# Kernel optimization log

Hardware: AMD Instinct MI355X
Metric: run time of the kernel (lower is better)

## Reference

```python
import jax, jax.numpy as jnp
import numpy as np

H, D = 8, 16          # heads, per-head dim (hidden=128)
N_NEWS, N_INTER, F_IN, C_OUT = 30000, 60000, 768, 4
HID = H * D


def setup_inputs() -> dict:
    key = jax.random.key(0)
    ks = jax.random.split(key, 20)
    s = lambda i, shape, sc=0.05: (jax.random.normal(ks[i], shape, dtype=jnp.float32) * sc)
    inp = {
        "x_news": jax.random.normal(ks[0], (N_NEWS, F_IN), dtype=jnp.float32),
        "x_inter": jax.random.normal(ks[1], (N_INTER, F_IN), dtype=jnp.float32),
        "edge_nn": jax.random.randint(ks[2], (2, 480000), 0, N_NEWS),
        "edge_in": jax.random.randint(ks[3], (2, 960000), 0, N_NEWS),
        # per-node-type input projections (HANConv.proj)
        "W_news": s(4, (F_IN, HID)), "b_news": jnp.zeros((HID,), jnp.float32),
        "W_inter": s(5, (F_IN, HID)), "b_inter": jnp.zeros((HID,), jnp.float32),
        # per-edge-type node-level attention vectors (lin_src / lin_dst)
        "a_src_nn": s(6, (H, D), 0.2), "a_dst_nn": s(7, (H, D), 0.2),
        "a_src_in": s(8, (H, D), 0.2), "a_dst_in": s(9, (H, D), 0.2),
        # semantic-level attention (k_lin, q)
        "Wk": s(10, (HID, HID)), "bk": jnp.zeros((HID,), jnp.float32),
        "q": s(11, (HID,), 0.2),
        # output head
        "W_out": s(12, (HID, C_OUT)), "b_out": jnp.zeros((C_OUT,), jnp.float32),
    }
    return inp


def _han_conv(h_src, h_dst, edge, a_src, a_dst, n_dst):
    # node-level (GAT-style) attention for one edge type
    asrc = (h_src * a_src).sum(-1)            # [Ns, H]
    adst = (h_dst * a_dst).sum(-1)            # [Nd, H]
    src, dst = edge[0], edge[1]
    e = jax.nn.leaky_relu(asrc[src] + adst[dst], negative_slope=0.2)   # [E, H]
    m = jax.ops.segment_max(e, dst, num_segments=n_dst)                # [Nd, H]
    m = jnp.where(jnp.isfinite(m), m, jnp.float32(0))
    ex = jnp.exp(e - m[dst])
    denom = jax.ops.segment_sum(ex, dst, num_segments=n_dst)
    alpha = ex / (denom[dst] + jnp.float32(1e-16))                     # [E, H]
    out = jax.ops.segment_sum(h_src[src] * alpha[:, :, None], dst, num_segments=n_dst)
    return jax.nn.relu(out.reshape(n_dst, H * D))                      # [Nd, HID]


def reference(x_news, x_inter, edge_nn, edge_in,
              W_news, b_news, W_inter, b_inter,
              a_src_nn, a_dst_nn, a_src_in, a_dst_in,
              Wk, bk, q, W_out, b_out):
    # per-node-type projection, reshape to heads
    h_news = (x_news @ W_news + b_news).reshape(-1, H, D)
    h_inter = (x_inter @ W_inter + b_inter).reshape(-1, H, D)
    # per-edge-type node-level attention conv (dst is always 'news')
    out_nn = _han_conv(h_news, h_news, edge_nn, a_src_nn, a_dst_nn, N_NEWS)
    out_in = _han_conv(h_inter, h_news, edge_in, a_src_in, a_dst_in, N_NEWS)
    # semantic-level attention across metapaths
    outs = jnp.stack([out_nn, out_in])                       # [2, N, HID]
    score = (q * jnp.tanh(outs @ Wk + bk).mean(axis=1)).sum(-1)   # [2]
    beta = jax.nn.softmax(score, axis=0)
    fused = (beta[:, None, None] * outs).sum(0)              # [N, HID]
    # head: ELU + (eval-mode dropout = identity) + Linear
    return jax.nn.elu(fused) @ W_out + b_out
```

## Files before the change

### kernel.cpp

```cpp
#include <hip/hip_runtime.h>
#include <hip/hip_bf16.h>

#define N_NODES   30000
#define F_IN      768
#define HID       128
#define NHEAD     8
#define C_OUT     4

typedef short short8_t __attribute__((ext_vector_type(8)));
typedef float float4_t __attribute__((ext_vector_type(4)));

__device__ __forceinline__ float b2f(short u) {
    union { unsigned int i; float f; } v;
    v.i = ((unsigned int)(unsigned short)u) << 16;
    return v.f;
}
__device__ __forceinline__ short f2s(float f) {
    __hip_bfloat16 h = __float2bfloat16(f);
    short s; __builtin_memcpy(&s, &h, 2); return s;
}

#define OFF_H_NEWS      0UL
#define OFF_H_INTER     7680000UL
#define OFF_OUT_NN      15360000UL
#define OFF_OUT_IN      23040000UL
#define OFF_ASRC_NN     30720000UL
#define OFF_ADST_NN     31680000UL
#define OFF_ASRC_IN     32640000UL
#define OFF_ADST_IN     33600000UL
#define OFF_WT_NEWS     34560000UL
#define OFF_WT_INTER    34756608UL
#define OFF_RS_NN       34953216UL
#define OFF_RS_IN       35073280UL
#define OFF_SORT_NN     35193344UL
#define OFF_SORT_IN     37113344UL
#define OFF_ZERO        40953344UL
#define OFF_DEG_NN      40953344UL
#define OFF_FILL_NN     41073408UL
#define OFF_DEG_IN      41193472UL
#define OFF_FILL_IN     41313536UL
#define OFF_SSUM        41433600UL
#define ZERO_BYTES      481280UL
#define OFF_BETA        41434624UL
#define OFF_FLAG        41434632UL
#define OFF_CPAR        41434640UL
#define OFF_WKT         41470496UL

#define CP_B_NEWS  0
#define CP_B_INTER 128
#define CP_ASRC_NN 256
#define CP_ADST_NN 384
#define CP_ASRC_IN 512
#define CP_ADST_IN 640
#define CP_WK      768
#define CP_BK      17152
#define CP_Q       17280
#define CP_WOUT    17408
#define CP_BOUT    17920
#define CP_TOTAL   17924

__global__ void detect_dtype(const unsigned int* __restrict__ x, int* __restrict__ flag) {
    __shared__ int cnt_s;
    if (threadIdx.x == 0) cnt_s = 0;
    __syncthreads();
    int sane = 0;
    for (int i = threadIdx.x; i < 16384; i += 256) {
        unsigned int lo = x[i] & 0xFFFFu;
        unsigned int ex = (lo >> 7) & 0xFFu;
        if ((ex >= 107u && ex <= 147u) || lo == 0u || lo == 0x8000u) sane++;
    }
    atomicAdd(&cnt_s, sane);
    __syncthreads();
    if (threadIdx.x == 0) *flag = (cnt_s > 8192) ? 1 : 0;
}

struct SmallParams {
    const void* src[11];
    int n[11];
    int dstoff[11];
};
__global__ void convert_small(SmallParams sp, short* __restrict__ dst,
                              const int* __restrict__ flag) {
    bool isbf = (*flag != 0);
    int idx = blockIdx.x * 256 + threadIdx.x;
    for (int s = 0; s < 11; ++s) {
        if (idx < sp.n[s]) {
            short v = isbf ? ((const short*)sp.src[s])[idx]
                           : f2s(((const float*)sp.src[s])[idx]);
            dst[sp.dstoff[s] + idx] = v;
            return;
        }
        idx -= sp.n[s];
    }
}

__global__ void transpose_w2(const void* __restrict__ Wn, const void* __restrict__ Wi,
                             short* __restrict__ WtN, short* __restrict__ WtI,
                             const int* __restrict__ flag) {
    bool isbf = (*flag != 0);
    const void* Wraw = blockIdx.y ? Wi : Wn;
    short* Wt        = blockIdx.y ? WtI : WtN;
    int idx = blockIdx.x * 256 + threadIdx.x;
    if (idx < F_IN * HID) {
        int n = idx / F_IN;
        int k = idx - n * F_IN;
        short v = isbf ? ((const short*)Wraw)[k * HID + n]
                       : f2s(((const float*)Wraw)[k * HID + n]);
        Wt[idx] = v;
    }
}

__global__ void transpose_wk(const short* __restrict__ cp, short* __restrict__ wkT) {
    int idx = blockIdx.x * 256 + threadIdx.x;
    if (idx < HID * HID) {
        int j = idx >> 7;
        int k = idx & 127;
        wkT[idx] = cp[CP_WK + k * HID + j];
    }
}

#define BK   32
#define LDK  40

__global__ __launch_bounds__(256) void proj_gemm2(
    const void* __restrict__ Xn, const void* __restrict__ Xi,
    const short* __restrict__ WtN, const short* __restrict__ WtI,
    const short* __restrict__ cp,
    short* __restrict__ Hn, short* __restrict__ Hi,
    int M, const int* __restrict__ flag)
{
    __shared__ __align__(16) short As[64 * LDK];
    __shared__ __align__(16) short Bs[128 * LDK];

    const bool isbf = (*flag != 0);
    const void* Xraw = blockIdx.y ? Xi : Xn;
    const short* Wt  = blockIdx.y ? WtI : WtN;
    const short* bias = cp + (blockIdx.y ? CP_B_INTER : CP_B_NEWS);
    short* Hout      = blockIdx.y ? Hi : Hn;

    int m0   = blockIdx.x * 64;
    int tid  = threadIdx.x;
    int lane = tid & 63;
    int wid  = tid >> 6;
    int quad = lane >> 4;
    int lm   = lane & 15;

    float4_t acc[8];
    #pragma unroll
    for (int c = 0; c < 8; ++c) acc[c] = (float4_t){0.f, 0.f, 0.f, 0.f};

    int sr  = tid >> 2;
    int skp = (tid & 3) * 8;

    for (int k0 = 0; k0 < F_IN; k0 += BK) {
        __syncthreads();
        {
            int gm = m0 + sr; if (gm >= M) gm = M - 1;
            short8_t av;
            if (isbf) {
                av = *(const short8_t*)((const short*)Xraw + (size_t)gm * F_IN + k0 + skp);
            } else {
                const float* xf = (const float*)Xraw + (size_t)gm * F_IN + k0 + skp;
                float4_t f0 = *(const float4_t*)xf;
                float4_t f1 = *(const float4_t*)(xf + 4);
                av[0] = f2s(f0[0]); av[1] = f2s(f0[1]); av[2] = f2s(f0[2]); av[3] = f2s(f0[3]);
                av[4] = f2s(f1[0]); av[5] = f2s(f1[1]); av[6] = f2s(f1[2]); av[7] = f2s(f1[3]);
            }
            *(short8_t*)(&As[sr * LDK + skp]) = av;
        }
        #pragma unroll
        for (int rep = 0; rep < 2; ++rep) {
            int r = sr + rep * 64;
            short8_t bv = *(const short8_t*)(Wt + (size_t)r * F_IN + k0 + skp);
            *(short8_t*)(&Bs[r * LDK + skp]) = bv;
        }
        __syncthreads();

        short8_t bfrag[8];
        #pragma unroll
        for (int c = 0; c < 8; ++c)
            bfrag[c] = *(const short8_t*)(&Bs[(c * 16 + lm) * LDK + quad * 8]);
        short8_t afrag = *(const short8_t*)(&As[(wid * 16 + lm) * LDK + quad * 8]);
        #pragma unroll
        for (int c = 0; c < 8; ++c)
            acc[c] = __builtin_amdgcn_mfma_f32_16x16x32_bf16(afrag, bfrag[c], acc[c], 0, 0, 0);
    }

    #pragma unroll
    for (int c = 0; c < 8; ++c)
        #pragma unroll
        for (int r = 0; r < 4; ++r) {
            int row = wid * 16 + quad * 4 + r;
            int gm = m0 + row;
            if (gm < M) {
                int col = c * 16 + lm;
                Hout[(size_t)gm * HID + col] = f2s(acc[c][r] + b2f(bias[col]));
            }
        }
}

__global__ __launch_bounds__(128) void head_dots(
    const short* __restrict__ Hnews, const short* __restrict__ Hinter,
    const short* __restrict__ cp,
    float* __restrict__ asrc_nn, float* __restrict__ adst_nn,
    float* __restrict__ asrc_in, float* __restrict__ adst_in)
{
    int n = blockIdx.x, tid = threadIdx.x;
    int h = tid >> 4, d = tid & 15;
    float hv  = b2f(Hnews[(size_t)n * HID + tid]);
    float hv2 = b2f(Hinter[(size_t)n * HID + tid]);
    float v0 = hv  * b2f(cp[CP_ASRC_NN + tid]);
    float v1 = hv  * b2f(cp[CP_ADST_NN + tid]);
    float v2 = hv2 * b2f(cp[CP_ASRC_IN + tid]);
    float v3 = hv  * b2f(cp[CP_ADST_IN + tid]);
    #pragma unroll
    for (int off = 8; off; off >>= 1) {
        v0 += __shfl_down(v0, off, 16);
        v1 += __shfl_down(v1, off, 16);
        v2 += __shfl_down(v2, off, 16);
        v3 += __shfl_down(v3, off, 16);
    }
    if (d == 0) {
        asrc_nn[n * NHEAD + h] = v0;
        adst_nn[n * NHEAD + h] = v1;
        asrc_in[n * NHEAD + h] = v2;
        adst_in[n * NHEAD + h] = v3;
    }
}

__global__ void count_deg2(const int* __restrict__ dnn, int Enn,
                           const int* __restrict__ din, int Ein,
                           int* __restrict__ deg_nn, int* __restrict__ deg_in) {
    int i = blockIdx.x * 256 + threadIdx.x;
    if (i < Enn) {
        int d = dnn[i];
        if (d >= 0 && d < N_NODES) atomicAdd(&deg_nn[d], 1);
    } else {
        int j = i - Enn;
        if (j < Ein) {
            int d = din[j];
            if (d >= 0 && d < N_NODES) atomicAdd(&deg_in[d], 1);
        }
    }
}

__global__ __launch_bounds__(256) void prefix_scan2(
    const int* __restrict__ deg_nn, int* __restrict__ rs_nn,
    const int* __restrict__ deg_in, int* __restrict__ rs_in, int n)
{
    const int* deg = blockIdx.x ? deg_in : deg_nn;
    int* row_start = blockIdx.x ? rs_in : rs_nn;
    __shared__ int psum[256];
    int tid = threadIdx.x;
    int chunk = (n + 255) / 256;
    int lo = tid * chunk;
    int hi = lo + chunk; if (hi > n) hi = n; if (lo > n) lo = n;
    int s = 0;
    for (int i = lo; i < hi; ++i) s += deg[i];
    psum[tid] = s;
    __syncthreads();
    for (int off = 1; off < 256; off <<= 1) {
        int v = (tid >= off) ? psum[tid - off] : 0;
        __syncthreads();
        psum[tid] += v;
        __syncthreads();
    }
    int base = tid ? psum[tid - 1] : 0;
    for (int i = lo; i < hi; ++i) { row_start[i] = base; base += deg[i]; }
    if (tid == 255) row_start[n] = psum[255];
}

__global__ void scatter_edges2(const int* __restrict__ enn, int Enn,
                               const int* __restrict__ ein, int Ein,
                               const int* __restrict__ rs_nn, int* __restrict__ fill_nn,
                               int* __restrict__ sort_nn,
                               const int* __restrict__ rs_in, int* __restrict__ fill_in,
                               int* __restrict__ sort_in) {
    int i = blockIdx.x * 256 + threadIdx.x;
    if (i < Enn) {
        int d = enn[Enn + i];
        if (d >= 0 && d < N_NODES) {
            int pos = rs_nn[d] + atomicAdd(&fill_nn[d], 1);
            if (pos >= 0 && pos < Enn) sort_nn[pos] = enn[i];
        }
    } else {
        int j = i - Enn;
        if (j < Ein) {
            int d = ein[Ein + j];
            if (d >= 0 && d < N_NODES) {
                int pos = rs_in[d] + atomicAdd(&fill_in[d], 1);
                if (pos >= 0 && pos < Ein) sort_in[pos] = ein[j];
            }
        }
    }
}

__global__ __launch_bounds__(256) void aggregate2(
    const short* __restrict__ Hnn, const short* __restrict__ Hin,
    const float* __restrict__ asrc_nn, const float* __restrict__ adst_nn,
    const float* __restrict__ asrc_in, const float* __restrict__ adst_in,
    const int* __restrict__ rs_nn, const int* __restrict__ rs_in,
    const int* __restrict__ sort_nn, const int* __restrict__ sort_in,
    short* __restrict__ out_nn, short* __restrict__ out_in)
{
    int tid = threadIdx.x, w = tid >> 6, lane = tid & 63;
    int type = blockIdx.y;
    const short* H    = type ? Hin : Hnn;
    const float* asrc = type ? asrc_in : asrc_nn;
    const float* adst = type ? adst_in : adst_nn;
    const int*   rs   = type ? rs_in : rs_nn;
    const int*   ss   = type ? sort_in : sort_nn;
    short* outb       = type ? out_in : out_nn;

    int dn = blockIdx.x * 4 + w;
    int start = rs[dn], end = rs[dn + 1];
    int head = lane >> 3;
    float adv = adst[dn * NHEAD + head];

    float den = 0.f, a0 = 0.f, a1 = 0.f;
    for (int base = start; base < end; base += 64) {
        int nb = end - base; if (nb > 64) nb = 64;
        int myidx = 0;
        if (base + lane < end) myidx = ss[base + lane];
        for (int j = 0; j < nb; ++j) {
            int s = __shfl(myidx, j, 64);
            s = (s < 0) ? 0 : (s >= N_NODES ? N_NODES - 1 : s);
            float e = asrc[s * NHEAD + head] + adv;
            e = fmaxf(e, 0.2f * e);
            e = fminf(e, 80.f);
            float ex = __expf(e);
            unsigned int hv = *(const unsigned int*)(H + (size_t)s * HID + lane * 2);
            den += ex;
            a0 += ex * b2f((short)(hv & 0xFFFFu));
            a1 += ex * b2f((short)(hv >> 16));
        }
    }
    float inv = 1.f / (den + 1e-16f);
    unsigned int lo16 = (unsigned short)f2s(fmaxf(a0 * inv, 0.f));
    unsigned int hi16 = (unsigned short)f2s(fmaxf(a1 * inv, 0.f));
    *(unsigned int*)(outb + (size_t)dn * HID + lane * 2) = lo16 | (hi16 << 16);
}

__global__ __launch_bounds__(256) void score_mfma(
    const short* __restrict__ out_nn, const short* __restrict__ out_in,
    const short* __restrict__ wkT, const short* __restrict__ cp,
    float* __restrict__ Ssum)
{
    __shared__ float col_s[HID];
    int tid  = threadIdx.x;
    int lane = tid & 63;
    int wid  = tid >> 6;
    int quad = lane >> 4;
    int lm   = lane & 15;
    const short* src = blockIdx.y ? out_in : out_nn;
    int m0 = blockIdx.x * 128;

    if (tid < HID) col_s[tid] = 0.f;
    __syncthreads();

    float4_t acc[2][8];
    #pragma unroll
    for (int i = 0; i < 2; ++i)
        #pragma unroll
        for (int c = 0; c < 8; ++c)
            acc[i][c] = (float4_t){0.f, 0.f, 0.f, 0.f};

    #pragma unroll
    for (int kc = 0; kc < 4; ++kc) {
        short8_t bfrag[8];
        #pragma unroll
        for (int c = 0; c < 8; ++c)
            bfrag[c] = *(const short8_t*)(wkT + (c * 16 + lm) * HID + kc * 32 + quad * 8);
        #pragma unroll
        for (int i = 0; i < 2; ++i) {
            int gm = m0 + wid * 32 + i * 16 + lm;
            if (gm >= N_NODES) gm = N_NODES - 1;
            short8_t afrag = *(const short8_t*)(src + (size_t)gm * HID + kc * 32 + quad * 8);
            #pragma unroll
            for (int c = 0; c < 8; ++c)
                acc[i][c] = __builtin_amdgcn_mfma_f32_16x16x32_bf16(afrag, bfrag[c], acc[i][c], 0, 0, 0);
        }
    }

    #pragma unroll
    for (int c = 0; c < 8; ++c) {
        int col = c * 16 + lm;
        float bkc = b2f(cp[CP_BK + col]);
        float lsum = 0.f;
        #pragma unroll
        for (int i = 0; i < 2; ++i)
            #pragma unroll
            for (int r = 0; r < 4; ++r) {
                int node = m0 + wid * 32 + i * 16 + quad * 4 + r;
                if (node < N_NODES) {
                    float a = acc[i][c][r] + bkc;
                    a = fminf(fmaxf(a, -15.f), 15.f);
                    float t = __expf(2.f * a);
                    lsum += (t - 1.f) / (t + 1.f);
                }
            }
        float v = lsum;
        v += __shfl_down(v, 32, 64);
        v += __shfl_down(v, 16, 64);
        if (quad == 0) atomicAdd(&col_s[col], v);
    }
    __syncthreads();
    if (tid < HID) atomicAdd(&Ssum[blockIdx.y * HID + tid], col_s[tid]);
}

__global__ __launch_bounds__(64) void beta_kernel(
    const float* __restrict__ Ssum, const short* __restrict__ cp, float* __restrict__ beta)
{
    int lane = threadIdx.x;
    float q0 = b2f(cp[CP_Q + lane]), q1 = b2f(cp[CP_Q + lane + 64]);
    float s0 = q0 * Ssum[lane] + q1 * Ssum[lane + 64];
    float s1 = q0 * Ssum[128 + lane] + q1 * Ssum[192 + lane];
    #pragma unroll
    for (int off = 32; off; off >>= 1) {
        s0 += __shfl_down(s0, off, 64);
        s1 += __shfl_down(s1, off, 64);
    }
    if (lane == 0) {
        float sc0 = s0 / (float)N_NODES;
        float sc1 = s1 / (float)N_NODES;
        float mx = fmaxf(sc0, sc1);
        float e0 = __expf(sc0 - mx), e1 = __expf(sc1 - mx);
        float inv = 1.f / (e0 + e1);
        beta[0] = e0 * inv;
        beta[1] = e1 * inv;
    }
}

__global__ __launch_bounds__(128) void final_out(
    const short* __restrict__ out_nn, const short* __restrict__ out_in,
    const float* __restrict__ beta, const short* __restrict__ cp,
    void* __restrict__ Yraw, const int* __restrict__ flag)
{
    __shared__ float partial[2][C_OUT];
    bool isbf = (*flag != 0);
    int n = blockIdx.x, tid = threadIdx.x, lane = tid & 63, w = tid >> 6;
    float b0 = beta[0], b1 = beta[1];
    float f = b0 * b2f(out_nn[(size_t)n * HID + tid]) + b1 * b2f(out_in[(size_t)n * HID + tid]);
    float e = (f > 0.f) ? f : expm1f(f);
    float p[C_OUT];
    #pragma unroll
    for (int c = 0; c < C_OUT; ++c) p[c] = e * b2f(cp[CP_WOUT + tid * C_OUT + c]);
    #pragma unroll
    for (int off = 32; off; off >>= 1)
        #pragma unroll
        for (int c = 0; c < C_OUT; ++c) p[c] += __shfl_down(p[c], off, 64);
    if (lane == 0)
        #pragma unroll
        for (int c = 0; c < C_OUT; ++c) partial[w][c] = p[c];
    __syncthreads();
    if (tid < C_OUT) {
        float r = partial[0][tid] + partial[1][tid] + b2f(cp[CP_BOUT + tid]);
        if (isbf) ((__hip_bfloat16*)Yraw)[n * C_OUT + tid] = __float2bfloat16(r);
        else      ((float*)Yraw)[n * C_OUT + tid] = r;
    }
}

extern "C" void kernel_launch(void* const* d_in, const int* in_sizes, int n_in,
                              void* d_out, int out_size, void* d_ws, size_t ws_size,
                              hipStream_t stream) {
    const void* x_news  = d_in[0];
    const void* x_inter = d_in[1];
    const int*  edge_nn = (const int*)d_in[2];
    const int*  edge_in = (const int*)d_in[3];

    int E_nn = in_sizes[2] / 2;
    int E_in = in_sizes[3] / 2;

    char* ws = (char*)d_ws;
    short* h_news  = (short*)(ws + OFF_H_NEWS);
    short* h_inter = (short*)(ws + OFF_H_INTER);
    short* out_nn  = (short*)(ws + OFF_OUT_NN);
    short* out_in  = (short*)(ws + OFF_OUT_IN);
    float* asrc_nn = (float*)(ws + OFF_ASRC_NN);
    float* adst_nn = (float*)(ws + OFF_ADST_NN);
    float* asrc_in = (float*)(ws + OFF_ASRC_IN);
    float* adst_in = (float*)(ws + OFF_ADST_IN);
    short* wt_news  = (short*)(ws + OFF_WT_NEWS);
    short* wt_inter = (short*)(ws + OFF_WT_INTER);
    int* rs_nn   = (int*)(ws + OFF_RS_NN);
    int* rs_in   = (int*)(ws + OFF_RS_IN);
    int* sort_nn = (int*)(ws + OFF_SORT_NN);
    int* sort_in = (int*)(ws + OFF_SORT_IN);
    int* deg_nn  = (int*)(ws + OFF_DEG_NN);
    int* fill_nn = (int*)(ws + OFF_FILL_NN);
    int* deg_in  = (int*)(ws + OFF_DEG_IN);
    int* fill_in = (int*)(ws + OFF_FILL_IN);
    float* Ssum  = (float*)(ws + OFF_SSUM);
    float* beta  = (float*)(ws + OFF_BETA);
    int*   flag  = (int*)(ws + OFF_FLAG);
    short* cp    = (short*)(ws + OFF_CPAR);
    short* wkT   = (short*)(ws + OFF_WKT);

    hipMemsetAsync(ws + OFF_ZERO, 0, ZERO_BYTES, stream);

    detect_dtype<<<1, 256, 0, stream>>>((const unsigned int*)x_news, flag);

    SmallParams sp;
    const int srcidx[11] = {5, 7, 8, 9, 10, 11, 12, 13, 14, 15, 16};
    const int ns[11]     = {128, 128, 128, 128, 128, 128, 16384, 128, 128, 512, 4};
    const int doff[11]   = {CP_B_NEWS, CP_B_INTER, CP_ASRC_NN, CP_ADST_NN, CP_ASRC_IN,
                            CP_ADST_IN, CP_WK, CP_BK, CP_Q, CP_WOUT, CP_BOUT};
    for (int i = 0; i < 11; ++i) { sp.src[i] = d_in[srcidx[i]]; sp.n[i] = ns[i]; sp.dstoff[i] = doff[i]; }
    convert_small<<<(CP_TOTAL + 255) / 256, 256, 0, stream>>>(sp, cp, flag);

    transpose_wk<<<(HID * HID + 255) / 256, 256, 0, stream>>>(cp, wkT);

    transpose_w2<<<dim3((F_IN * HID + 255) / 256, 2), 256, 0, stream>>>(
        d_in[4], d_in[6], wt_news, wt_inter, flag);

    proj_gemm2<<<dim3((N_NODES + 63) / 64, 2), 256, 0, stream>>>(
        x_news, x_inter, wt_news, wt_inter, cp, h_news, h_inter, N_NODES, flag);

    head_dots<<<N_NODES, 128, 0, stream>>>(h_news, h_inter, cp,
        asrc_nn, adst_nn, asrc_in, adst_in);

    count_deg2<<<(E_nn + E_in + 255) / 256, 256, 0, stream>>>(
        edge_nn + E_nn, E_nn, edge_in + E_in, E_in, deg_nn, deg_in);

    prefix_scan2<<<2, 256, 0, stream>>>(deg_nn, rs_nn, deg_in, rs_in, N_NODES);

    scatter_edges2<<<(E_nn + E_in + 255) / 256, 256, 0, stream>>>(
        edge_nn, E_nn, edge_in, E_in, rs_nn, fill_nn, sort_nn, rs_in, fill_in, sort_in);

    aggregate2<<<dim3(N_NODES / 4, 2), 256, 0, stream>>>(
        h_news, h_inter, asrc_nn, adst_nn, asrc_in, adst_in,
        rs_nn, rs_in, sort_nn, sort_in, out_nn, out_in);

    score_mfma<<<dim3((N_NODES + 127) / 128, 2), 256, 0, stream>>>(out_nn, out_in, wkT, cp, Ssum);
    beta_kernel<<<1, 64, 0, stream>>>(Ssum, cp, beta);

    final_out<<<N_NODES, 128, 0, stream>>>(out_nn, out_in, beta, cp, d_out, flag);
}
```

Before: 703.8 us.

## Fuse prep, projection, head dots and degree count; merge beta into score

```diff
diff --git a/kernel.cpp b/kernel.cpp
--- a/kernel.cpp
+++ b/kernel.cpp
@@ -9,6 +9,7 @@
 
 typedef short short8_t __attribute__((ext_vector_type(8)));
 typedef float float4_t __attribute__((ext_vector_type(4)));
+typedef int   int4_t   __attribute__((ext_vector_type(4)));
 
 __device__ __forceinline__ float b2f(short u) {
     union { unsigned int i; float f; } v;
@@ -40,11 +41,12 @@
 #define OFF_DEG_IN      41193472UL
 #define OFF_FILL_IN     41313536UL
 #define OFF_SSUM        41433600UL
-#define ZERO_BYTES      481280UL
-#define OFF_BETA        41434624UL
-#define OFF_FLAG        41434632UL
-#define OFF_CPAR        41434640UL
-#define OFF_WKT         41470496UL
+#define OFF_CNT         41434624UL
+#define ZERO_BYTES      481296UL
+#define OFF_BETA        41434640UL
+#define OFF_FLAG        41434648UL
+#define OFF_CPAR        41434656UL
+#define OFF_WKT         41470512UL
 
 #define CP_B_NEWS  0
 #define CP_B_INTER 128
@@ -59,12 +61,23 @@
 #define CP_BOUT    17920
 #define CP_TOTAL   17924
 
+#define PREP_CONV_BLOCKS 7
+#define PREP_TW_BLOCKS   384
+#define PREP_WK_BLOCKS   64
+#define PREP_ZERO_BLOCKS 118
+#define PREP_B0 PREP_CONV_BLOCKS
+#define PREP_B1 (PREP_B0 + 2*PREP_TW_BLOCKS)
+#define PREP_B2 (PREP_B1 + PREP_WK_BLOCKS)
+#define PREP_TOTAL (PREP_B2 + PREP_ZERO_BLOCKS)
+
+#define GEMM_BX 469
+
 __global__ void detect_dtype(const unsigned int* __restrict__ x, int* __restrict__ flag) {
     __shared__ int cnt_s;
     if (threadIdx.x == 0) cnt_s = 0;
     __syncthreads();
     int sane = 0;
-    for (int i = threadIdx.x; i < 16384; i += 256) {
+    for (int i = threadIdx.x; i < 16384; i += 1024) {
         unsigned int lo = x[i] & 0xFFFFu;
         unsigned int ex = (lo >> 7) & 0xFFu;
         if ((ex >= 107u && ex <= 147u) || lo == 0u || lo == 0x8000u) sane++;
@@ -75,70 +88,100 @@
 }
 
 struct SmallParams {
-    const void* src[11];
-    int n[11];
-    int dstoff[11];
+    const void* src[10];
+    int n[10];
+    int dstoff[10];
 };
-__global__ void convert_small(SmallParams sp, short* __restrict__ dst,
-                              const int* __restrict__ flag) {
-    bool isbf = (*flag != 0);
-    int idx = blockIdx.x * 256 + threadIdx.x;
-    for (int s = 0; s < 11; ++s) {
-        if (idx < sp.n[s]) {
-            short v = isbf ? ((const short*)sp.src[s])[idx]
-                           : f2s(((const float*)sp.src[s])[idx]);
-            dst[sp.dstoff[s] + idx] = v;
-            return;
-        }
-        idx -= sp.n[s];
-    }
-}
-
-__global__ void transpose_w2(const void* __restrict__ Wn, const void* __restrict__ Wi,
-                             short* __restrict__ WtN, short* __restrict__ WtI,
-                             const int* __restrict__ flag) {
-    bool isbf = (*flag != 0);
-    const void* Wraw = blockIdx.y ? Wi : Wn;
-    short* Wt        = blockIdx.y ? WtI : WtN;
-    int idx = blockIdx.x * 256 + threadIdx.x;
-    if (idx < F_IN * HID) {
-        int n = idx / F_IN;
-        int k = idx - n * F_IN;
-        short v = isbf ? ((const short*)Wraw)[k * HID + n]
-                       : f2s(((const float*)Wraw)[k * HID + n]);
-        Wt[idx] = v;
-    }
-}
-
-__global__ void transpose_wk(const short* __restrict__ cp, short* __restrict__ wkT) {
-    int idx = blockIdx.x * 256 + threadIdx.x;
-    if (idx < HID * HID) {
-        int j = idx >> 7;
-        int k = idx & 127;
-        wkT[idx] = cp[CP_WK + k * HID + j];
+
+__global__ void prep(SmallParams sp, short* __restrict__ cp,
+                     const void* __restrict__ Wn, const void* __restrict__ Wi,
+                     const void* __restrict__ Wkraw,
+                     short* __restrict__ WtN, short* __restrict__ WtI,
+                     short* __restrict__ wkT,
+                     char* __restrict__ zbase,
+                     const int* __restrict__ flag) {
+    const bool isbf = (*flag != 0);
+    int b = blockIdx.x, tid = threadIdx.x;
+    if (b < PREP_B0) {
+        int idx = b * 256 + tid;
+        for (int s = 0; s < 10; ++s) {
+            if (idx < sp.n[s]) {
+                short v = isbf ? ((const short*)sp.src[s])[idx]
+                               : f2s(((const float*)sp.src[s])[idx]);
+                cp[sp.dstoff[s] + idx] = v;
+                return;
+            }
+            idx -= sp.n[s];
+        }
+    } else if (b < PREP_B1) {
+        int bb = b - PREP_B0;
+        int ty = bb >= PREP_TW_BLOCKS;
+        const void* Wraw = ty ? Wi : Wn;
+        short* Wt        = ty ? WtI : WtN;
+        int idx = (bb - ty * PREP_TW_BLOCKS) * 256 + tid;
+        if (idx < F_IN * HID) {
+            int n = idx / F_IN;
+            int k = idx - n * F_IN;
+            Wt[idx] = isbf ? ((const short*)Wraw)[k * HID + n]
+                           : f2s(((const float*)Wraw)[k * HID + n]);
+        }
+    } else if (b < PREP_B2) {
+        int idx = (b - PREP_B1) * 256 + tid;
+        if (idx < HID * HID) {
+            int j = idx >> 7;
+            int k = idx & 127;
+            wkT[idx] = isbf ? ((const short*)Wkraw)[k * HID + j]
+                            : f2s(((const float*)Wkraw)[k * HID + j]);
+        }
+    } else {
+        size_t off = ((size_t)(b - PREP_B2) * 256 + tid) * 16;
+        if (off < ZERO_BYTES) *(int4_t*)(zbase + off) = (int4_t){0, 0, 0, 0};
     }
 }
 
 #define BK   32
 #define LDK  40
 
-__global__ __launch_bounds__(256) void proj_gemm2(
+__global__ __launch_bounds__(256) void proj_count(
     const void* __restrict__ Xn, const void* __restrict__ Xi,
     const short* __restrict__ WtN, const short* __restrict__ WtI,
     const short* __restrict__ cp,
     short* __restrict__ Hn, short* __restrict__ Hi,
+    float* __restrict__ asrc_nn, float* __restrict__ adst_nn,
+    float* __restrict__ asrc_in, float* __restrict__ adst_in,
+    const int* __restrict__ dnn, int Enn,
+    const int* __restrict__ din, int Ein,
+    int* __restrict__ deg_nn, int* __restrict__ deg_in,
     int M, const int* __restrict__ flag)
 {
     __shared__ __align__(16) short As[64 * LDK];
     __shared__ __align__(16) short Bs[128 * LDK];
 
+    int b = blockIdx.x;
+    if (b >= 2 * GEMM_BX) {
+        int i = (b - 2 * GEMM_BX) * 256 + threadIdx.x;
+        if (i < Enn) {
+            int d = dnn[i];
+            if ((unsigned)d < (unsigned)N_NODES) atomicAdd(&deg_nn[d], 1);
+        } else {
+            int j = i - Enn;
+            if (j < Ein) {
+                int d = din[j];
+                if ((unsigned)d < (unsigned)N_NODES) atomicAdd(&deg_in[d], 1);
+            }
+        }
+        return;
+    }
+
     const bool isbf = (*flag != 0);
-    const void* Xraw = blockIdx.y ? Xi : Xn;
-    const short* Wt  = blockIdx.y ? WtI : WtN;
-    const short* bias = cp + (blockIdx.y ? CP_B_INTER : CP_B_NEWS);
-    short* Hout      = blockIdx.y ? Hi : Hn;
-
-    int m0   = blockIdx.x * 64;
+    int ty = b >= GEMM_BX;
+    int bx = b - ty * GEMM_BX;
+    const void* Xraw = ty ? Xi : Xn;
+    const short* Wt  = ty ? WtI : WtN;
+    const short* bias = cp + (ty ? CP_B_INTER : CP_B_NEWS);
+    short* Hout      = ty ? Hi : Hn;
+
+    int m0   = bx * 64;
     int tid  = threadIdx.x;
     int lane = tid & 63;
     int wid  = tid >> 6;
@@ -186,60 +229,43 @@
             acc[c] = __builtin_amdgcn_mfma_f32_16x16x32_bf16(afrag, bfrag[c], acc[c], 0, 0, 0);
     }
 
+    const short* aw0 = cp + (ty ? CP_ASRC_IN : CP_ASRC_NN);
+    const short* aw1 = cp + CP_ADST_NN;
+    const short* aw2 = cp + CP_ADST_IN;
+
     #pragma unroll
-    for (int c = 0; c < 8; ++c)
+    for (int c = 0; c < 8; ++c) {
+        int col = c * 16 + lm;
+        float bv = b2f(bias[col]);
+        float w0 = b2f(aw0[col]);
+        float w1 = b2f(aw1[col]);
+        float w2 = b2f(aw2[col]);
         #pragma unroll
         for (int r = 0; r < 4; ++r) {
-            int row = wid * 16 + quad * 4 + r;
-            int gm = m0 + row;
-            if (gm < M) {
-                int col = c * 16 + lm;
-                Hout[(size_t)gm * HID + col] = f2s(acc[c][r] + b2f(bias[col]));
+            int gm = m0 + wid * 16 + quad * 4 + r;
+            bool ok = gm < M;
+            float hval = acc[c][r] + bv;
+            if (ok) Hout[(size_t)gm * HID + col] = f2s(hval);
+            if (ty == 0) {
+                float d0 = hval * w0, d1 = hval * w1, d2 = hval * w2;
+                #pragma unroll
+                for (int off = 1; off < 16; off <<= 1) {
+                    d0 += __shfl_xor(d0, off, 16);
+                    d1 += __shfl_xor(d1, off, 16);
+                    d2 += __shfl_xor(d2, off, 16);
+                }
+                if (lm == 0 && ok) {
+                    asrc_nn[gm * NHEAD + c] = d0;
+                    adst_nn[gm * NHEAD + c] = d1;
+                    adst_in[gm * NHEAD + c] = d2;
+                }
+            } else {
+                float d0 = hval * w0;
+                #pragma unroll
+                for (int off = 1; off < 16; off <<= 1)
+                    d0 += __shfl_xor(d0, off, 16);
+                if (lm == 0 && ok) asrc_in[gm * NHEAD + c] = d0;
             }
-        }
-}
-
-__global__ __launch_bounds__(128) void head_dots(
-    const short* __restrict__ Hnews, const short* __restrict__ Hinter,
-    const short* __restrict__ cp,
-    float* __restrict__ asrc_nn, float* __restrict__ adst_nn,
-    float* __restrict__ asrc_in, float* __restrict__ adst_in)
-{
-    int n = blockIdx.x, tid = threadIdx.x;
-    int h = tid >> 4, d = tid & 15;
-    float hv  = b2f(Hnews[(size_t)n * HID + tid]);
-    float hv2 = b2f(Hinter[(size_t)n * HID + tid]);
-    float v0 = hv  * b2f(cp[CP_ASRC_NN + tid]);
-    float v1 = hv  * b2f(cp[CP_ADST_NN + tid]);
-    float v2 = hv2 * b2f(cp[CP_ASRC_IN + tid]);
-    float v3 = hv  * b2f(cp[CP_ADST_IN + tid]);
-    #pragma unroll
-    for (int off = 8; off; off >>= 1) {
-        v0 += __shfl_down(v0, off, 16);
-        v1 += __shfl_down(v1, off, 16);
-        v2 += __shfl_down(v2, off, 16);
-        v3 += __shfl_down(v3, off, 16);
-    }
-    if (d == 0) {
-        asrc_nn[n * NHEAD + h] = v0;
-        adst_nn[n * NHEAD + h] = v1;
-        asrc_in[n * NHEAD + h] = v2;
-        adst_in[n * NHEAD + h] = v3;
-    }
-}
-
-__global__ void count_deg2(const int* __restrict__ dnn, int Enn,
-                           const int* __restrict__ din, int Ein,
-                           int* __restrict__ deg_nn, int* __restrict__ deg_in) {
-    int i = blockIdx.x * 256 + threadIdx.x;
-    if (i < Enn) {
-        int d = dnn[i];
-        if (d >= 0 && d < N_NODES) atomicAdd(&deg_nn[d], 1);
-    } else {
-        int j = i - Enn;
-        if (j < Ein) {
-            int d = din[j];
-            if (d >= 0 && d < N_NODES) atomicAdd(&deg_in[d], 1);
         }
     }
 }
@@ -316,23 +342,48 @@
     int start = rs[dn], end = rs[dn + 1];
     int head = lane >> 3;
     float adv = adst[dn * NHEAD + head];
+    const short* Hl = H + lane * 2;
 
     float den = 0.f, a0 = 0.f, a1 = 0.f;
     for (int base = start; base < end; base += 64) {
         int nb = end - base; if (nb > 64) nb = 64;
         int myidx = 0;
-        if (base + lane < end) myidx = ss[base + lane];
-        for (int j = 0; j < nb; ++j) {
-            int s = __shfl(myidx, j, 64);
-            s = (s < 0) ? 0 : (s >= N_NODES ? N_NODES - 1 : s);
-            float e = asrc[s * NHEAD + head] + adv;
-            e = fmaxf(e, 0.2f * e);
-            e = fminf(e, 80.f);
-            float ex = __expf(e);
-            unsigned int hv = *(const unsigned int*)(H + (size_t)s * HID + lane * 2);
-            den += ex;
-            a0 += ex * b2f((short)(hv & 0xFFFFu));
-            a1 += ex * b2f((short)(hv >> 16));
+        if (base + lane < end) {
+            int t = ss[base + lane];
+            myidx = (t < 0) ? 0 : (t >= N_NODES ? N_NODES - 1 : t);
+        }
+        int j = 0;
+        for (; j + 2 <= nb; j += 2) {
+            int s0 = __shfl(myidx, j, 64);
+            int s1 = __shfl(myidx, j + 1, 64);
+            float v0 = asrc[s0 * NHEAD + head];
+            float v1 = asrc[s1 * NHEAD + head];
+            unsigned int q0 = *(const unsigned int*)(Hl + (size_t)s0 * HID);
+            unsigned int q1 = *(const unsigned int*)(Hl + (size_t)s1 * HID);
+            float e0 = v0 + adv, e1 = v1 + adv;
+            e0 = fmaxf(e0, 0.2f * e0); e1 = fmaxf(e1, 0.2f * e1);
+            e0 = fminf(e0, 80.f);      e1 = fminf(e1, 80.f);
+            float x0 = __expf(e0), x1 = __expf(e1);
+            union { unsigned int u; float f; } cl0, ch0, cl1, ch1;
+            cl0.u = q0 << 16; ch0.u = q0 & 0xFFFF0000u;
+            cl1.u = q1 << 16; ch1.u = q1 & 0xFFFF0000u;
+            den += x0; den += x1;
+            a0 = fmaf(x0, cl0.f, a0); a0 = fmaf(x1, cl1.f, a0);
+            a1 = fmaf(x0, ch0.f, a1); a1 = fmaf(x1, ch1.f, a1);
+        }
+        if (j < nb) {
+            int s0 = __shfl(myidx, j, 64);
+            float v0 = asrc[s0 * NHEAD + head];
+            unsigned int q0 = *(const unsigned int*)(Hl + (size_t)s0 * HID);
+            float e0 = v0 + adv;
+            e0 = fmaxf(e0, 0.2f * e0);
+            e0 = fminf(e0, 80.f);
+            float x0 = __expf(e0);
+            union { unsigned int u; float f; } cl0, ch0;
+            cl0.u = q0 << 16; ch0.u = q0 & 0xFFFF0000u;
+            den += x0;
+            a0 = fmaf(x0, cl0.f, a0);
+            a1 = fmaf(x0, ch0.f, a1);
         }
     }
     float inv = 1.f / (den + 1e-16f);
@@ -344,9 +395,11 @@
 __global__ __launch_bounds__(256) void score_mfma(
     const short* __restrict__ out_nn, const short* __restrict__ out_in,
     const short* __restrict__ wkT, const short* __restrict__ cp,
-    float* __restrict__ Ssum)
+    float* __restrict__ Ssum, int* __restrict__ done_cnt,
+    float* __restrict__ beta, int total_blocks)
 {
     __shared__ float col_s[HID];
+    __shared__ int lastflag;
     int tid  = threadIdx.x;
     int lane = tid & 63;
     int wid  = tid >> 6;
@@ -406,57 +459,73 @@
     }
     __syncthreads();
     if (tid < HID) atomicAdd(&Ssum[blockIdx.y * HID + tid], col_s[tid]);
-}
-
-__global__ __launch_bounds__(64) void beta_kernel(
-    const float* __restrict__ Ssum, const short* __restrict__ cp, float* __restrict__ beta)
-{
-    int lane = threadIdx.x;
-    float q0 = b2f(cp[CP_Q + lane]), q1 = b2f(cp[CP_Q + lane + 64]);
-    float s0 = q0 * Ssum[lane] + q1 * Ssum[lane + 64];
-    float s1 = q0 * Ssum[128 + lane] + q1 * Ssum[192 + lane];
-    #pragma unroll
-    for (int off = 32; off; off >>= 1) {
-        s0 += __shfl_down(s0, off, 64);
-        s1 += __shfl_down(s1, off, 64);
-    }
-    if (lane == 0) {
-        float sc0 = s0 / (float)N_NODES;
-        float sc1 = s1 / (float)N_NODES;
-        float mx = fmaxf(sc0, sc1);
-        float e0 = __expf(sc0 - mx), e1 = __expf(sc1 - mx);
-        float inv = 1.f / (e0 + e1);
-        beta[0] = e0 * inv;
-        beta[1] = e1 * inv;
-    }
-}
-
-__global__ __launch_bounds__(128) void final_out(
+    __syncthreads();
+
+    if (tid == 0) {
+        __threadfence();
+        int old = atomicAdd(done_cnt, 1);
+        lastflag = (old == total_blocks - 1) ? 1 : 0;
+    }
+    __syncthreads();
+    if (lastflag && tid < 64) {
+        float s00 = atomicAdd(&Ssum[tid], 0.f);
+        float s01 = atomicAdd(&Ssum[tid + 64], 0.f);
+        float s10 = atomicAdd(&Ssum[128 + tid], 0.f);
+        float s11 = atomicAdd(&Ssum[192 + tid], 0.f);
+        float q0 = b2f(cp[CP_Q + tid]), q1 = b2f(cp[CP_Q + tid + 64]);
+        float v0 = q0 * s00 + q1 * s01;
+        float v1 = q0 * s10 + q1 * s11;
+        #pragma unroll
+        for (int off = 32; off; off >>= 1) {
+            v0 += __shfl_down(v0, off, 64);
+            v1 += __shfl_down(v1, off, 64);
+        }
+        if (tid == 0) {
+            float sc0 = v0 / (float)N_NODES;
+            float sc1 = v1 / (float)N_NODES;
+            float mx = fmaxf(sc0, sc1);
+            float e0 = __expf(sc0 - mx), e1 = __expf(sc1 - mx);
+            float inv = 1.f / (e0 + e1);
+            beta[0] = e0 * inv;
+            beta[1] = e1 * inv;
+        }
+    }
+}
+
+__global__ __launch_bounds__(256) void final_out(
     const short* __restrict__ out_nn, const short* __restrict__ out_in,
     const float* __restrict__ beta, const short* __restrict__ cp,
     void* __restrict__ Yraw, const int* __restrict__ flag)
 {
-    __shared__ float partial[2][C_OUT];
     bool isbf = (*flag != 0);
-    int n = blockIdx.x, tid = threadIdx.x, lane = tid & 63, w = tid >> 6;
+    int tid = threadIdx.x, lane = tid & 63, w = tid >> 6;
+    int n = blockIdx.x * 4 + w;
     float b0 = beta[0], b1 = beta[1];
-    float f = b0 * b2f(out_nn[(size_t)n * HID + tid]) + b1 * b2f(out_in[(size_t)n * HID + tid]);
-    float e = (f > 0.f) ? f : expm1f(f);
+    unsigned int u0 = *(const unsigned int*)(out_nn + (size_t)n * HID + lane * 2);
+    unsigned int u1 = *(const unsigned int*)(out_in + (size_t)n * HID + lane * 2);
+    union { unsigned int u; float f; } t;
+    t.u = u0 << 16;          float f0 = b0 * t.f;
+    t.u = u0 & 0xFFFF0000u;  float f1 = b0 * t.f;
+    t.u = u1 << 16;          f0 += b1 * t.f;
+    t.u = u1 & 0xFFFF0000u;  f1 += b1 * t.f;
+    float e0 = (f0 > 0.f) ? f0 : expm1f(f0);
+    float e1 = (f1 > 0.f) ? f1 : expm1f(f1);
+    int c0 = lane * 2, c1 = lane * 2 + 1;
     float p[C_OUT];
     #pragma unroll
-    for (int c = 0; c < C_OUT; ++c) p[c] = e * b2f(cp[CP_WOUT + tid * C_OUT + c]);
+    for (int c = 0; c < C_OUT; ++c)
+        p[c] = e0 * b2f(cp[CP_WOUT + c0 * C_OUT + c]) + e1 * b2f(cp[CP_WOUT + c1 * C_OUT + c]);
     #pragma unroll
     for (int off = 32; off; off >>= 1)
         #pragma unroll
         for (int c = 0; c < C_OUT; ++c) p[c] += __shfl_down(p[c], off, 64);
-    if (lane == 0)
-        #pragma unroll
-        for (int c = 0; c < C_OUT; ++c) partial[w][c] = p[c];
-    __syncthreads();
-    if (tid < C_OUT) {
-        float r = partial[0][tid] + partial[1][tid] + b2f(cp[CP_BOUT + tid]);
-        if (isbf) ((__hip_bfloat16*)Yraw)[n * C_OUT + tid] = __float2bfloat16(r);
-        else      ((float*)Yraw)[n * C_OUT + tid] = r;
+    if (lane == 0) {
+        #pragma unroll
+        for (int c = 0; c < C_OUT; ++c) {
+            float r = p[c] + b2f(cp[CP_BOUT + c]);
+            if (isbf) ((__hip_bfloat16*)Yraw)[n * C_OUT + c] = __float2bfloat16(r);
+            else      ((float*)Yraw)[n * C_OUT + c] = r;
+        }
     }
 }
 
@@ -491,48 +560,43 @@
     int* deg_in  = (int*)(ws + OFF_DEG_IN);
     int* fill_in = (int*)(ws + OFF_FILL_IN);
     float* Ssum  = (float*)(ws + OFF_SSUM);
+    int*   dcnt  = (int*)(ws + OFF_CNT);
     float* beta  = (float*)(ws + OFF_BETA);
     int*   flag  = (int*)(ws + OFF_FLAG);
     short* cp    = (short*)(ws + OFF_CPAR);
     short* wkT   = (short*)(ws + OFF_WKT);
 
-    hipMemsetAsync(ws + OFF_ZERO, 0, ZERO_BYTES, stream);
-
-    detect_dtype<<<1, 256, 0, stream>>>((const unsigned int*)x_news, flag);
+    detect_dtype<<<1, 1024, 0, stream>>>((const unsigned int*)x_news, flag);
 
     SmallParams sp;
-    const int srcidx[11] = {5, 7, 8, 9, 10, 11, 12, 13, 14, 15, 16};
-    const int ns[11]     = {128, 128, 128, 128, 128, 128, 16384, 128, 128, 512, 4};
-    const int doff[11]   = {CP_B_NEWS, CP_B_INTER, CP_ASRC_NN, CP_ADST_NN, CP_ASRC_IN,
-                            CP_ADST_IN, CP_WK, CP_BK, CP_Q, CP_WOUT, CP_BOUT};
-    for (int i = 0; i < 11; ++i) { sp.src[i] = d_in[srcidx[i]]; sp.n[i] = ns[i]; sp.dstoff[i] = doff[i]; }
-    convert_small<<<(CP_TOTAL + 255) / 256, 256, 0, stream>>>(sp, cp, flag);
-
-    transpose_wk<<<(HID * HID + 255) / 256, 256, 0, stream>>>(cp, wkT);
-
-    transpose_w2<<<dim3((F_IN * HID + 255) / 256, 2), 256, 0, stream>>>(
-        d_in[4], d_in[6], wt_news, wt_inter, flag);
-
-    proj_gemm2<<<dim3((N_NODES + 63) / 64, 2), 256, 0, stream>>>(
-        x_news, x_inter, wt_news, wt_inter, cp, h_news, h_inter, N_NODES, flag);
-
-    head_dots<<<N_NODES, 128, 0, stream>>>(h_news, h_inter, cp,
-        asrc_nn, adst_nn, asrc_in, adst_in);
-
-    count_deg2<<<(E_nn + E_in + 255) / 256, 256, 0, stream>>>(
-        edge_nn + E_nn, E_nn, edge_in + E_in, E_in, deg_nn, deg_in);
+    const int srcidx[10] = {5, 7, 8, 9, 10, 11, 13, 14, 15, 16};
+    const int ns[10]     = {128, 128, 128, 128, 128, 128, 128, 128, 512, 4};
+    const int doff[10]   = {CP_B_NEWS, CP_B_INTER, CP_ASRC_NN, CP_ADST_NN, CP_ASRC_IN,
+                            CP_ADST_IN, CP_BK, CP_Q, CP_WOUT, CP_BOUT};
+    for (int i = 0; i < 10; ++i) { sp.src[i] = d_in[srcidx[i]]; sp.n[i] = ns[i]; sp.dstoff[i] = doff[i]; }
+
+    prep<<<PREP_TOTAL, 256, 0, stream>>>(sp, cp, d_in[4], d_in[6], d_in[12],
+                                         wt_news, wt_inter, wkT, ws + OFF_ZERO, flag);
+
+    int cnt_blocks = (E_nn + E_in + 255) / 256;
+    proj_count<<<2 * GEMM_BX + cnt_blocks, 256, 0, stream>>>(
+        x_news, x_inter, wt_news, wt_inter, cp, h_news, h_inter,
+        asrc_nn, adst_nn, asrc_in, adst_in,
+        edge_nn + E_nn, E_nn, edge_in + E_in, E_in, deg_nn, deg_in,
+        N_NODES, flag);
 
     prefix_scan2<<<2, 256, 0, stream>>>(deg_nn, rs_nn, deg_in, rs_in, N_NODES);
 
-    scatter_edges2<<<(E_nn + E_in + 255) / 256, 256, 0, stream>>>(
+    scatter_edges2<<<cnt_blocks, 256, 0, stream>>>(
         edge_nn, E_nn, edge_in, E_in, rs_nn, fill_nn, sort_nn, rs_in, fill_in, sort_in);
 
     aggregate2<<<dim3(N_NODES / 4, 2), 256, 0, stream>>>(
         h_news, h_inter, asrc_nn, adst_nn, asrc_in, adst_in,
         rs_nn, rs_in, sort_nn, sort_in, out_nn, out_in);
 
-    score_mfma<<<dim3((N_NODES + 127) / 128, 2), 256, 0, stream>>>(out_nn, out_in, wkT, cp, Ssum);
-    beta_kernel<<<1, 64, 0, stream>>>(Ssum, cp, beta);
-
-    final_out<<<N_NODES, 128, 0, stream>>>(out_nn, out_in, beta, cp, d_out, flag);
-}
+    int score_bx = (N_NODES + 127) / 128;
+    score_mfma<<<dim3(score_bx, 2), 256, 0, stream>>>(
+        out_nn, out_in, wkT, cp, Ssum, dcnt, beta, 2 * score_bx);
+
+    final_out<<<N_NODES / 4, 256, 0, stream>>>(out_nn, out_in, beta, cp, d_out, flag);
+}
```

Measured after the change: 584.9 us. -16.9%, faster.
